# Optimization experiments

Hardware: AMD Instinct MI355X
Metric: run time of the kernel (lower is better)

The kernel has to match this reference:

```python
import jax, jax.numpy as jnp
import numpy as np

B, S, D, H, E = 4, 2048, 1024, 4096, 8
TOP_K = 2


def setup_inputs() -> dict:
    key = jax.random.key(0)
    k = jax.random.split(key, 7)
    scale_in = 1.0 / np.sqrt(D)
    scale_h = 1.0 / np.sqrt(H)
    return {
        "x": jax.random.normal(k[0], (B, S, D), jnp.float32),
        "Wr": jax.random.normal(k[1], (D, E), jnp.float32) * scale_in,
        "br": jnp.zeros((E,), jnp.float32),
        "W1": jax.random.normal(k[2], (E, D, H), jnp.float32) * scale_in,
        "b1": jnp.zeros((E, H), jnp.float32),
        "W2": jax.random.normal(k[3], (E, H, D), jnp.float32) * scale_h,
        "b2": jnp.zeros((E, D), jnp.float32),
    }


def reference(x, Wr, br, W1, b1, W2, b2):
    # Router: softmax over experts, then top-k and renormalize.
    routing = jax.nn.softmax(x @ Wr + br, axis=-1)            # [B,S,E]
    topk_vals, topk_idx = jax.lax.top_k(routing, TOP_K)        # [B,S,K]
    topk_norm = topk_vals / jnp.sum(topk_vals, axis=-1, keepdims=True)
    # Scatter normalized top-k weights back to a dense [B,S,E] gate.
    gate = jnp.sum(jax.nn.one_hot(topk_idx, E, dtype=x.dtype) * topk_norm[..., None], axis=2)  # [B,S,E]
    # Per-expert FFN over all tokens (original's dense masked loop; masked-out
    # tokens have gate==0 so zeroing inputs is mathematically equivalent).
    h = jax.nn.relu(jnp.einsum("bsd,edh->ebsh", x, W1) + b1[:, None, None, :])  # [E,B,S,H]
    y = jnp.einsum("ebsh,ehd->ebsd", h, W2) + b2[:, None, None, :]              # [E,B,S,D]
    out = jnp.einsum("ebsd,bse->bsd", y, gate)                                   # [B,S,D]
    return out
```

## Files before the change

kernel.cpp:

```cpp
#include <hip/hip_runtime.h>
#include <stdint.h>

typedef unsigned short u16;
typedef __attribute__((ext_vector_type(8))) short s8bf;
typedef __attribute__((ext_vector_type(4))) float f32x4;

#define N_TOK 8192
#define DIM   1024
#define HID   4096
#define NE    8
#define MAX_SLOTS 17408
#define MAX_TILES 160
#define LSTR  152
#define TSTR  264

#define OFF_W1T  ((size_t)0)
#define OFF_Y    ((size_t)0)
#define OFF_W2T  ((size_t)67108864)
#define OFF_XB   ((size_t)134217728)
#define OFF_H    ((size_t)150994944)
#define OFF_TOS  ((size_t)293601280)
#define OFF_SOT  ((size_t)293670912)
#define OFF_TKI  ((size_t)293740544)
#define OFF_TKW  ((size_t)293806080)
#define OFF_CNT  ((size_t)293871616)
#define OFF_POF  ((size_t)293871680)
#define OFF_CUR  ((size_t)293871744)
#define OFF_NT   ((size_t)293871808)
#define OFF_TE   ((size_t)293871872)
#define OFF_TS   ((size_t)293872896)

__device__ __forceinline__ u16 f2b(float v) {
  union { float f; uint32_t u; } c; c.f = v;
  uint32_t u = c.u;
  return (u16)((u + 0x7FFFu + ((u >> 16) & 1u)) >> 16);
}
__device__ __forceinline__ float b2f(u16 b) {
  union { uint32_t u; float f; } c; c.u = ((uint32_t)b) << 16; return c.f;
}

typedef const __attribute__((address_space(1))) uint32_t* gp32;
typedef __attribute__((address_space(3))) uint32_t* lp32;
__device__ __forceinline__ void gl_lds16(const u16* g, u16* l) {
  __builtin_amdgcn_global_load_lds((gp32)(const void*)g, (lp32)(void*)l, 16, 0, 0);
}

__global__ __launch_bounds__(256) void transpose_to_bf16(
    const float* __restrict__ in, u16* __restrict__ out, int R, int C) {
  __shared__ u16 L[64 * TSTR];
  int tiles_c = C >> 6, tiles_r = R >> 8;
  int per = tiles_c * tiles_r;
  int e = blockIdx.x / per, t = blockIdx.x % per;
  int tr = t / tiles_c, tc = t % tiles_c;
  const float* ip = in + (size_t)e * R * C + (size_t)(tr * 256) * C + tc * 64;
  u16* op = out + (size_t)e * R * C + (size_t)(tc * 64) * R + tr * 256;
  const int tid = threadIdx.x;
  const int c = tid & 63;
  const int rb0 = (tid >> 6) * 8;
  #pragma unroll
  for (int p = 0; p < 8; p++) {
    int rb = p * 32 + rb0;
    u16 tmp[8];
    #pragma unroll
    for (int j = 0; j < 8; j++) tmp[j] = f2b(ip[(size_t)(rb + j) * C + c]);
    *(uint4*)&L[c * TSTR + rb] = *(const uint4*)tmp;
  }
  __syncthreads();
  const int s = tid & 31, ocb = tid >> 5;
  #pragma unroll
  for (int p = 0; p < 8; p++) {
    int oc = p * 8 + ocb;
    uint4 v = *(const uint4*)&L[oc * TSTR + s * 8];
    *(uint4*)&op[(size_t)oc * R + s * 8] = v;
  }
}

__global__ __launch_bounds__(256) void convert_x(const float* __restrict__ x,
                                                 u16* __restrict__ xb) {
  size_t i = ((size_t)blockIdx.x * 256 + threadIdx.x) * 8;
  float4 v0 = *(const float4*)(x + i);
  float4 v1 = *(const float4*)(x + i + 4);
  u16 o[8] = {f2b(v0.x), f2b(v0.y), f2b(v0.z), f2b(v0.w),
              f2b(v1.x), f2b(v1.y), f2b(v1.z), f2b(v1.w)};
  *(uint4*)(xb + i) = *(const uint4*)o;
}

__global__ __launch_bounds__(256) void router_kernel(
    const float* __restrict__ x, const float* __restrict__ Wr,
    const float* __restrict__ br, int* __restrict__ tki, float* __restrict__ tkw,
    int* __restrict__ counts) {
  int wave = threadIdx.x >> 6, lane = threadIdx.x & 63;
  int t = blockIdx.x * 4 + wave;
  const float* xr = x + (size_t)t * DIM;
  float acc[8] = {0.f, 0.f, 0.f, 0.f, 0.f, 0.f, 0.f, 0.f};
  #pragma unroll
  for (int i = 0; i < 16; i++) {
    int d = lane + i * 64;
    float xv = xr[d];
    float4 wa = *(const float4*)(Wr + d * 8);
    float4 wb = *(const float4*)(Wr + d * 8 + 4);
    acc[0] += xv * wa.x; acc[1] += xv * wa.y; acc[2] += xv * wa.z; acc[3] += xv * wa.w;
    acc[4] += xv * wb.x; acc[5] += xv * wb.y; acc[6] += xv * wb.z; acc[7] += xv * wb.w;
  }
  #pragma unroll
  for (int e = 0; e < 8; e++)
    #pragma unroll
    for (int off = 32; off >= 1; off >>= 1)
      acc[e] += __shfl_xor(acc[e], off, 64);
  if (lane == 0) {
    float l[8];
    #pragma unroll
    for (int e = 0; e < 8; e++) l[e] = acc[e] + br[e];
    float l0 = -1e30f; int i0 = 0;
    #pragma unroll
    for (int e = 0; e < 8; e++) if (l[e] > l0) { l0 = l[e]; i0 = e; }
    float l1 = -1e30f; int i1 = 0;
    #pragma unroll
    for (int e = 0; e < 8; e++) if (e != i0 && l[e] > l1) { l1 = l[e]; i1 = e; }
    float w0 = 1.f / (1.f + expf(l1 - l0));
    tki[t * 2] = i0; tki[t * 2 + 1] = i1;
    tkw[t * 2] = w0; tkw[t * 2 + 1] = 1.f - w0;
    atomicAdd(&counts[i0], 1);
    atomicAdd(&counts[i1], 1);
  }
}

__global__ void plan_kernel(const int* __restrict__ counts, int* __restrict__ poff,
                            int* __restrict__ cursor, int* __restrict__ ntiles,
                            int* __restrict__ tile_e, int* __restrict__ tile_s0) {
  int e = threadIdx.x;
  if (e < NE) {
    int po = 0, tb = 0;
    for (int i = 0; i < e; i++) {
      int tl = (counts[i] + 127) >> 7;
      po += tl << 7; tb += tl;
    }
    poff[e] = po;
    cursor[e] = 0;
    int tl = (counts[e] + 127) >> 7;
    for (int j = 0; j < tl; j++) { tile_e[tb + j] = e; tile_s0[tb + j] = po + j * 128; }
    if (e == NE - 1) ntiles[0] = tb + tl;
  }
}

__global__ __launch_bounds__(256) void scatter_kernel(
    const int* __restrict__ tki, const int* __restrict__ poff,
    int* __restrict__ cursor, int* __restrict__ token_of_slot,
    int* __restrict__ slot_of_token) {
  int t = blockIdx.x * 256 + threadIdx.x;
  #pragma unroll
  for (int k = 0; k < 2; k++) {
    int e = tki[t * 2 + k];
    int r = atomicAdd(&cursor[e], 1);
    int s = poff[e] + r;
    token_of_slot[s] = t;
    slot_of_token[t * 2 + k] = s;
  }
}

template <int MODE>
__global__ __launch_bounds__(256) void moe_gemm(
    const u16* __restrict__ A, const u16* __restrict__ Bt,
    const float* __restrict__ bias, u16* __restrict__ Hout,
    const int* __restrict__ tile_e, const int* __restrict__ tile_s0,
    const int* __restrict__ ntiles, const int* __restrict__ token_of_slot,
    int K, int N, int NB) {
  const int nblk = blockIdx.x % NB;
  const int tileid = blockIdx.x / NB;
  if (tileid >= ntiles[0]) return;
  const int e = tile_e[tileid];
  const int slot0 = tile_s0[tileid];
  const int n0 = nblk * 128;

  __shared__ u16 SM[128 * LSTR];
  u16* lA[2] = {SM, SM + 4096};
  u16* lB[2] = {SM + 8192, SM + 12288};

  const int tid = threadIdx.x;
  const int lane = tid & 63;
  const int wave = tid >> 6;
  const int wm = wave >> 1, wn = wave & 1;

  const int r0 = tid >> 2, r1 = r0 + 64;
  const int c8 = (tid & 3) * 8;
  int arow0, arow1;
  if (MODE == 1) {
    int t0 = token_of_slot[slot0 + r0]; arow0 = t0 < 0 ? 0 : t0;
    int t1 = token_of_slot[slot0 + r1]; arow1 = t1 < 0 ? 0 : t1;
  } else {
    arow0 = slot0 + r0; arow1 = slot0 + r1;
  }
  const u16* aP0 = A + (size_t)arow0 * K + c8;
  const u16* aP1 = A + (size_t)arow1 * K + c8;
  const u16* bE = Bt + (size_t)e * N * K;
  const u16* bP0 = bE + (size_t)(n0 + r0) * K + c8;
  const u16* bP1 = bE + (size_t)(n0 + r1) * K + c8;

  f32x4 acc[4][4];
  #pragma unroll
  for (int i = 0; i < 4; i++)
    #pragma unroll
    for (int j = 0; j < 4; j++) acc[i][j] = (f32x4){0.f, 0.f, 0.f, 0.f};

  const int qk = (lane >> 4) * 8;
  const int am = (lane & 15);

  for (int kb = 0; kb < K; kb += 64) {
    #pragma unroll
    for (int h = 0; h < 2; h++) {
      int ko = kb + h * 32;
      gl_lds16(aP0 + ko, lA[h] + wave * 512);
      gl_lds16(aP1 + ko, lA[h] + 2048 + wave * 512);
      gl_lds16(bP0 + ko, lB[h] + wave * 512);
      gl_lds16(bP1 + ko, lB[h] + 2048 + wave * 512);
    }
    __syncthreads();
    #pragma unroll
    for (int h = 0; h < 2; h++) {
      s8bf af[4], bf[4];
      #pragma unroll
      for (int mt = 0; mt < 4; mt++)
        af[mt] = *(const s8bf*)&lA[h][(wm * 64 + mt * 16 + am) * 32 + qk];
      #pragma unroll
      for (int nt = 0; nt < 4; nt++)
        bf[nt] = *(const s8bf*)&lB[h][(wn * 64 + nt * 16 + am) * 32 + qk];
      #pragma unroll
      for (int mt = 0; mt < 4; mt++)
        #pragma unroll
        for (int nt = 0; nt < 4; nt++)
          acc[mt][nt] = __builtin_amdgcn_mfma_f32_16x16x32_bf16(af[mt], bf[nt],
                                                                acc[mt][nt], 0, 0, 0);
    }
    __syncthreads();
  }

  const int colq = lane & 15;
  const int rq = (lane >> 4) * 4;
  #pragma unroll
  for (int nt = 0; nt < 4; nt++) {
    int lcol = wn * 64 + nt * 16 + colq;
    float bv = bias[(size_t)e * N + n0 + lcol];
    #pragma unroll
    for (int mt = 0; mt < 4; mt++) {
      int rowbase = wm * 64 + mt * 16 + rq;
      #pragma unroll
      for (int r = 0; r < 4; r++) {
        float v = acc[mt][nt][r] + bv;
        if (MODE == 1) v = fmaxf(v, 0.f);
        SM[(rowbase + r) * LSTR + lcol] = f2b(v);
      }
    }
  }
  __syncthreads();
  #pragma unroll
  for (int k = 0; k < 8; k++) {
    int ch = k * 256 + tid;
    int row = ch >> 4;
    int cp = (ch & 15) * 8;
    uint4 v = *(const uint4*)&SM[row * LSTR + cp];
    *(uint4*)&Hout[(size_t)(slot0 + row) * N + n0 + cp] = v;
  }
}

__global__ __launch_bounds__(256) void combine_kernel(
    const u16* __restrict__ y, const int* __restrict__ sot,
    const float* __restrict__ tkw, float* __restrict__ out) {
  int wave = threadIdx.x >> 6, lane = threadIdx.x & 63;
  int t = blockIdx.x * 4 + wave;
  int s0 = sot[t * 2], s1 = sot[t * 2 + 1];
  float w0 = tkw[t * 2], w1 = tkw[t * 2 + 1];
  const u16* y0 = y + (size_t)s0 * DIM;
  const u16* y1 = y + (size_t)s1 * DIM;
  float* op = out + (size_t)t * DIM;
  #pragma unroll
  for (int i = 0; i < 4; i++) {
    int d = i * 256 + lane * 4;
    uint2 a = *(const uint2*)(y0 + d);
    uint2 b = *(const uint2*)(y1 + d);
    float4 o;
    o.x = w0 * b2f((u16)(a.x & 0xFFFF)) + w1 * b2f((u16)(b.x & 0xFFFF));
    o.y = w0 * b2f((u16)(a.x >> 16))    + w1 * b2f((u16)(b.x >> 16));
    o.z = w0 * b2f((u16)(a.y & 0xFFFF)) + w1 * b2f((u16)(b.y & 0xFFFF));
    o.w = w0 * b2f((u16)(a.y >> 16))    + w1 * b2f((u16)(b.y >> 16));
    *(float4*)(op + d) = o;
  }
}

extern "C" void kernel_launch(void* const* d_in, const int* in_sizes, int n_in,
                              void* d_out, int out_size, void* d_ws, size_t ws_size,
                              hipStream_t stream) {
  const float* x  = (const float*)d_in[0];
  const float* Wr = (const float*)d_in[1];
  const float* br = (const float*)d_in[2];
  const float* W1 = (const float*)d_in[3];
  const float* b1 = (const float*)d_in[4];
  const float* W2 = (const float*)d_in[5];
  const float* b2 = (const float*)d_in[6];
  float* out = (float*)d_out;
  char* ws = (char*)d_ws;

  u16*   W1t  = (u16*)(ws + OFF_W1T);
  u16*   W2t  = (u16*)(ws + OFF_W2T);
  u16*   ybuf = (u16*)(ws + OFF_Y);
  u16*   xb   = (u16*)(ws + OFF_XB);
  u16*   hbuf = (u16*)(ws + OFF_H);
  int*   tos  = (int*)(ws + OFF_TOS);
  int*   sot  = (int*)(ws + OFF_SOT);
  int*   tki  = (int*)(ws + OFF_TKI);
  float* tkw  = (float*)(ws + OFF_TKW);
  int*   cnt  = (int*)(ws + OFF_CNT);
  int*   pof  = (int*)(ws + OFF_POF);
  int*   cur  = (int*)(ws + OFF_CUR);
  int*   nt   = (int*)(ws + OFF_NT);
  int*   te   = (int*)(ws + OFF_TE);
  int*   ts   = (int*)(ws + OFF_TS);

  hipMemsetAsync(tos, 0xFF, (size_t)MAX_SLOTS * sizeof(int), stream);
  hipMemsetAsync(cnt, 0, 8 * sizeof(int), stream);

  transpose_to_bf16<<<dim3(NE * (DIM / 256) * (HID / 64)), 256, 0, stream>>>(W1, W1t, DIM, HID);
  transpose_to_bf16<<<dim3(NE * (HID / 256) * (DIM / 64)), 256, 0, stream>>>(W2, W2t, HID, DIM);
  convert_x<<<dim3(N_TOK * DIM / (256 * 8)), 256, 0, stream>>>(x, xb);
  router_kernel<<<dim3(N_TOK / 4), 256, 0, stream>>>(x, Wr, br, tki, tkw, cnt);
  plan_kernel<<<dim3(1), 64, 0, stream>>>(cnt, pof, cur, nt, te, ts);
  scatter_kernel<<<dim3(N_TOK / 256), 256, 0, stream>>>(tki, pof, cur, tos, sot);

  moe_gemm<1><<<dim3((MAX_SLOTS / 128) * (HID / 128)), 256, 0, stream>>>(
      xb, W1t, b1, hbuf, te, ts, nt, tos, DIM, HID, HID / 128);
  moe_gemm<2><<<dim3((MAX_SLOTS / 128) * (DIM / 128)), 256, 0, stream>>>(
      hbuf, W2t, b2, ybuf, te, ts, nt, tos, HID, DIM, DIM / 128);
  combine_kernel<<<dim3(N_TOK / 4), 256, 0, stream>>>(ybuf, sot, tkw, out);
}
```

Baseline: 1.005 ms.

## Rewrite MoE GEMM with 128x256 tiles, swizzled LDS and interleaved prefetch pipeline

The expert GEMM kernel moves to 512-thread blocks computing 128x256 output tiles with 64-wide K steps. Global-to-LDS loads now go into XOR-swizzled double buffers and are issued two K-steps ahead. They are interleaved between MFMA groups with barriers, explicit vmcnt waits and s_setprio raised around the math. The aim is to hide global memory latency, cut LDS bank conflicts and improve reuse of the A tile across a wider N. The costs are more LDS per block (96 KB, which may limit occupancy), more registers, and a row-staged epilogue with extra barriers.

```diff
diff --git a/kernel.cpp b/kernel.cpp
--- a/kernel.cpp
+++ b/kernel.cpp
@@ -11,7 +11,6 @@
 #define NE    8
 #define MAX_SLOTS 17408
 #define MAX_TILES 160
-#define LSTR  152
 #define TSTR  264
 
 #define OFF_W1T  ((size_t)0)
@@ -159,42 +158,77 @@
 }
 
 template <int MODE>
-__global__ __launch_bounds__(256) void moe_gemm(
+__global__ __launch_bounds__(512, 2) void moe_gemm(
     const u16* __restrict__ A, const u16* __restrict__ Bt,
     const float* __restrict__ bias, u16* __restrict__ Hout,
     const int* __restrict__ tile_e, const int* __restrict__ tile_s0,
     const int* __restrict__ ntiles, const int* __restrict__ token_of_slot,
     int K, int N, int NB) {
+  __shared__ u16 SM[49152];
+
   const int nblk = blockIdx.x % NB;
   const int tileid = blockIdx.x / NB;
   if (tileid >= ntiles[0]) return;
   const int e = tile_e[tileid];
   const int slot0 = tile_s0[tileid];
-  const int n0 = nblk * 128;
-
-  __shared__ u16 SM[128 * LSTR];
-  u16* lA[2] = {SM, SM + 4096};
-  u16* lB[2] = {SM + 8192, SM + 12288};
+  const int n0 = nblk * 256;
+  const int T = K >> 6;
 
   const int tid = threadIdx.x;
   const int lane = tid & 63;
   const int wave = tid >> 6;
-  const int wm = wave >> 1, wn = wave & 1;
-
-  const int r0 = tid >> 2, r1 = r0 + 64;
-  const int c8 = (tid & 3) * 8;
-  int arow0, arow1;
-  if (MODE == 1) {
-    int t0 = token_of_slot[slot0 + r0]; arow0 = t0 < 0 ? 0 : t0;
-    int t1 = token_of_slot[slot0 + r1]; arow1 = t1 < 0 ? 0 : t1;
-  } else {
-    arow0 = slot0 + r0; arow1 = slot0 + r1;
-  }
-  const u16* aP0 = A + (size_t)arow0 * K + c8;
-  const u16* aP1 = A + (size_t)arow1 * K + c8;
+  const int wm = wave >> 2;
+  const int wn = wave & 3;
+
+  const int srow = tid >> 3;
+  const int sslot = tid & 7;
+  const u16* aB[2];
+  #pragma unroll
+  for (int l = 0; l < 2; l++) {
+    int row = l * 64 + srow;
+    int scol = (sslot ^ (row & 7)) * 8;
+    int arow;
+    if (MODE == 1) { int t0 = token_of_slot[slot0 + row]; arow = t0 < 0 ? 0 : t0; }
+    else arow = slot0 + row;
+    aB[l] = A + (size_t)arow * K + scol;
+  }
   const u16* bE = Bt + (size_t)e * N * K;
-  const u16* bP0 = bE + (size_t)(n0 + r0) * K + c8;
-  const u16* bP1 = bE + (size_t)(n0 + r1) * K + c8;
+  const u16* bB[4];
+  #pragma unroll
+  for (int l = 0; l < 4; l++) {
+    int row = l * 64 + srow;
+    int scol = (sslot ^ (row & 7)) * 8;
+    bB[l] = bE + (size_t)(n0 + row) * K + scol;
+  }
+
+  const int colq = lane & 15;
+  float bv[4];
+  #pragma unroll
+  for (int n = 0; n < 4; n++) bv[n] = bias[(size_t)e * N + n0 + wn * 64 + n * 16 + colq];
+  asm volatile("s_waitcnt vmcnt(0)" ::: "memory");
+
+  const int wb = wave * 64;
+  #pragma unroll
+  for (int tt = 0; tt < 2; tt++) {
+    const int kq = tt * 64;
+    u16* LA = SM + tt * 8192;
+    u16* LB = SM + 16384 + tt * 16384;
+    gl_lds16(aB[0] + kq, LA + wb * 8);
+    gl_lds16(aB[1] + kq, LA + (512 + wb) * 8);
+    gl_lds16(bB[0] + kq, LB + wb * 8);
+    gl_lds16(bB[1] + kq, LB + (512 + wb) * 8);
+    gl_lds16(bB[2] + kq, LB + (1024 + wb) * 8);
+    gl_lds16(bB[3] + kq, LB + (1536 + wb) * 8);
+  }
+  asm volatile("s_waitcnt vmcnt(6)" ::: "memory");
+  __builtin_amdgcn_s_barrier();
+
+  const int q4 = lane >> 4;
+  const int sx = lane & 7;
+  const int sk0 = (q4 ^ sx) * 8;
+  const int sk1 = sk0 ^ 32;
+  const int aOff = (wm * 64 + (lane & 15)) * 64;
+  const int bOff = (wn * 64 + (lane & 15)) * 64;
 
   f32x4 acc[4][4];
   #pragma unroll
@@ -202,63 +236,102 @@
     #pragma unroll
     for (int j = 0; j < 4; j++) acc[i][j] = (f32x4){0.f, 0.f, 0.f, 0.f};
 
-  const int qk = (lane >> 4) * 8;
-  const int am = (lane & 15);
-
-  for (int kb = 0; kb < K; kb += 64) {
-    #pragma unroll
-    for (int h = 0; h < 2; h++) {
-      int ko = kb + h * 32;
-      gl_lds16(aP0 + ko, lA[h] + wave * 512);
-      gl_lds16(aP1 + ko, lA[h] + 2048 + wave * 512);
-      gl_lds16(bP0 + ko, lB[h] + wave * 512);
-      gl_lds16(bP1 + ko, lB[h] + 2048 + wave * 512);
+  int kk = 128;
+  for (int t = 0; t < T; ++t) {
+    const int cb = t & 1;
+    const u16* LA = SM + cb * 8192;
+    const u16* LB = SM + 16384 + cb * 16384;
+    u16* sLA = SM + cb * 8192;
+    u16* sLB = SM + 16384 + cb * 16384;
+    s8bf af[4][2], bf[4][2];
+
+    #pragma unroll
+    for (int m = 0; m < 4; m++) af[m][0] = *(const s8bf*)&LA[aOff + m * 1024 + sk0];
+    #pragma unroll
+    for (int n = 0; n < 4; n++) bf[n][0] = *(const s8bf*)&LB[bOff + n * 1024 + sk0];
+    __builtin_amdgcn_s_barrier();
+    __builtin_amdgcn_s_setprio(1);
+    #pragma unroll
+    for (int m = 0; m < 4; m++)
+      #pragma unroll
+      for (int n = 0; n < 2; n++)
+        acc[m][n] = __builtin_amdgcn_mfma_f32_16x16x32_bf16(af[m][0], bf[n][0], acc[m][n], 0, 0, 0);
+    __builtin_amdgcn_s_setprio(0);
+    __builtin_amdgcn_s_barrier();
+
+    #pragma unroll
+    for (int m = 0; m < 4; m++) af[m][1] = *(const s8bf*)&LA[aOff + m * 1024 + sk1];
+    #pragma unroll
+    for (int n = 0; n < 4; n++) bf[n][1] = *(const s8bf*)&LB[bOff + n * 1024 + sk1];
+    __builtin_amdgcn_s_barrier();
+    __builtin_amdgcn_s_setprio(1);
+    #pragma unroll
+    for (int m = 0; m < 4; m++)
+      #pragma unroll
+      for (int n = 2; n < 4; n++)
+        acc[m][n] = __builtin_amdgcn_mfma_f32_16x16x32_bf16(af[m][0], bf[n][0], acc[m][n], 0, 0, 0);
+    __builtin_amdgcn_s_setprio(0);
+    asm volatile("s_waitcnt lgkmcnt(0)" ::: "memory");
+    __builtin_amdgcn_s_barrier();
+
+    if (t + 2 < T) {
+      gl_lds16(aB[0] + kk, sLA + wb * 8);
+      gl_lds16(aB[1] + kk, sLA + (512 + wb) * 8);
+      gl_lds16(bB[0] + kk, sLB + wb * 8);
+    }
+    __builtin_amdgcn_s_barrier();
+    __builtin_amdgcn_s_setprio(1);
+    #pragma unroll
+    for (int m = 0; m < 4; m++)
+      #pragma unroll
+      for (int n = 0; n < 2; n++)
+        acc[m][n] = __builtin_amdgcn_mfma_f32_16x16x32_bf16(af[m][1], bf[n][1], acc[m][n], 0, 0, 0);
+    __builtin_amdgcn_s_setprio(0);
+    __builtin_amdgcn_s_barrier();
+
+    if (t + 2 < T) {
+      gl_lds16(bB[1] + kk, sLB + (512 + wb) * 8);
+      gl_lds16(bB[2] + kk, sLB + (1024 + wb) * 8);
+      gl_lds16(bB[3] + kk, sLB + (1536 + wb) * 8);
+    }
+    __builtin_amdgcn_s_barrier();
+    __builtin_amdgcn_s_setprio(1);
+    #pragma unroll
+    for (int m = 0; m < 4; m++)
+      #pragma unroll
+      for (int n = 2; n < 4; n++)
+        acc[m][n] = __builtin_amdgcn_mfma_f32_16x16x32_bf16(af[m][1], bf[n][1], acc[m][n], 0, 0, 0);
+    __builtin_amdgcn_s_setprio(0);
+    if (t < T - 2)       asm volatile("s_waitcnt vmcnt(6)" ::: "memory");
+    else if (t == T - 2) asm volatile("s_waitcnt vmcnt(0)" ::: "memory");
+    __builtin_amdgcn_s_barrier();
+    kk += 64;
+  }
+
+  #pragma unroll
+  for (int m = 0; m < 4; m++) {
+    __syncthreads();
+    const int rbase = wm * 16 + ((lane >> 4) << 2);
+    #pragma unroll
+    for (int n = 0; n < 4; n++) {
+      const int lcol = wn * 64 + n * 16 + colq;
+      #pragma unroll
+      for (int r = 0; r < 4; r++) {
+        float v = acc[m][n][r] + bv[n];
+        if (MODE == 1) v = fmaxf(v, 0.f);
+        SM[(rbase + r) * 264 + lcol] = f2b(v);
+      }
     }
     __syncthreads();
     #pragma unroll
-    for (int h = 0; h < 2; h++) {
-      s8bf af[4], bf[4];
-      #pragma unroll
-      for (int mt = 0; mt < 4; mt++)
-        af[mt] = *(const s8bf*)&lA[h][(wm * 64 + mt * 16 + am) * 32 + qk];
-      #pragma unroll
-      for (int nt = 0; nt < 4; nt++)
-        bf[nt] = *(const s8bf*)&lB[h][(wn * 64 + nt * 16 + am) * 32 + qk];
-      #pragma unroll
-      for (int mt = 0; mt < 4; mt++)
-        #pragma unroll
-        for (int nt = 0; nt < 4; nt++)
-          acc[mt][nt] = __builtin_amdgcn_mfma_f32_16x16x32_bf16(af[mt], bf[nt],
-                                                                acc[mt][nt], 0, 0, 0);
+    for (int it = 0; it < 2; it++) {
+      const int idx = it * 512 + tid;
+      const int rl = idx >> 5;
+      const int c16 = (idx & 31) * 8;
+      const int grow = (rl < 16) ? (m * 16 + rl) : (48 + m * 16 + rl);
+      uint4 v = *(const uint4*)&SM[rl * 264 + c16];
+      *(uint4*)&Hout[(size_t)(slot0 + grow) * N + n0 + c16] = v;
     }
-    __syncthreads();
-  }
-
-  const int colq = lane & 15;
-  const int rq = (lane >> 4) * 4;
-  #pragma unroll
-  for (int nt = 0; nt < 4; nt++) {
-    int lcol = wn * 64 + nt * 16 + colq;
-    float bv = bias[(size_t)e * N + n0 + lcol];
-    #pragma unroll
-    for (int mt = 0; mt < 4; mt++) {
-      int rowbase = wm * 64 + mt * 16 + rq;
-      #pragma unroll
-      for (int r = 0; r < 4; r++) {
-        float v = acc[mt][nt][r] + bv;
-        if (MODE == 1) v = fmaxf(v, 0.f);
-        SM[(rowbase + r) * LSTR + lcol] = f2b(v);
-      }
-    }
-  }
-  __syncthreads();
-  #pragma unroll
-  for (int k = 0; k < 8; k++) {
-    int ch = k * 256 + tid;
-    int row = ch >> 4;
-    int cp = (ch & 15) * 8;
-    uint4 v = *(const uint4*)&SM[row * LSTR + cp];
-    *(uint4*)&Hout[(size_t)(slot0 + row) * N + n0 + cp] = v;
   }
 }
 
@@ -325,9 +398,9 @@
   plan_kernel<<<dim3(1), 64, 0, stream>>>(cnt, pof, cur, nt, te, ts);
   scatter_kernel<<<dim3(N_TOK / 256), 256, 0, stream>>>(tki, pof, cur, tos, sot);
 
-  moe_gemm<1><<<dim3((MAX_SLOTS / 128) * (HID / 128)), 256, 0, stream>>>(
-      xb, W1t, b1, hbuf, te, ts, nt, tos, DIM, HID, HID / 128);
-  moe_gemm<2><<<dim3((MAX_SLOTS / 128) * (DIM / 128)), 256, 0, stream>>>(
-      hbuf, W2t, b2, ybuf, te, ts, nt, tos, HID, DIM, DIM / 128);
+  moe_gemm<1><<<dim3((MAX_SLOTS / 128) * (HID / 256)), 512, 0, stream>>>(
+      xb, W1t, b1, hbuf, te, ts, nt, tos, DIM, HID, HID / 256);
+  moe_gemm<2><<<dim3((MAX_SLOTS / 128) * (DIM / 256)), 512, 0, stream>>>(
+      hbuf, W2t, b2, ybuf, te, ts, nt, tos, HID, DIM, DIM / 256);
   combine_kernel<<<dim3(N_TOK / 4), 256, 0, stream>>>(ybuf, sot, tkw, out);
 }
```

Measured after the change: 1.041 ms. 3.6% more time.
